# Optimization experiments

Hardware: AMD Instinct MI355X
Metric: run time of the kernel (lower is better)

The kernel has to match this reference:

```python
import jax, jax.numpy as jnp
import numpy as np

SCALE = 64 ** 0.5  # module hard-codes sqrt(64), independent of output_dim


def setup_inputs() -> dict:
    key = jax.random.key(0)
    kx, kw = jax.random.split(key)
    x = jax.random.normal(kx, (8, 2048, 768), dtype=jnp.float32)
    kernel = jax.random.normal(kw, (3, 768, 768), dtype=jnp.float32) * 0.02
    return {"x": x, "kernel": kernel}


def reference(x, kernel):
    # x: [b, s, d]; kernel: [3, d, o]
    q = jnp.einsum('bsd,do->bso', x, kernel[0])
    k = jnp.einsum('bsd,do->bso', x, kernel[1])
    v = jnp.einsum('bsd,do->bso', x, kernel[2])
    scores = jnp.einsum('bso,bto->bst', q, k) / SCALE  # [b, s, s]
    attn = jax.nn.softmax(scores, axis=-1)
    return jnp.einsum('bst,bto->bso', attn, v)
```

## Files before the change

### kernel.cpp

```cpp
#include <hip/hip_runtime.h>

typedef unsigned short u16;
typedef unsigned int   u32;
typedef __bf16  bf16x8 __attribute__((ext_vector_type(8)));
typedef float   f32x4  __attribute__((ext_vector_type(4)));

__device__ __forceinline__ u16 f2bf(float f) {
  u32 u = __builtin_bit_cast(u32, f);
  u += 0x7FFFu + ((u >> 16) & 1u);
  return (u16)(u >> 16);
}
__device__ __forceinline__ u16 to_bits(float f) { return f2bf(f); }
__device__ __forceinline__ u16 to_bits(u16 u)   { return u; }
__device__ __forceinline__ u32 pack2(float lo, float hi) {
  return (u32)f2bf(lo) | ((u32)f2bf(hi) << 16);
}

__device__ __forceinline__ void gload_lds16(const u16* g, u16* l) {
  __builtin_amdgcn_global_load_lds((const __attribute__((address_space(1))) void*)g,
                                   (__attribute__((address_space(3))) void*)l,
                                   16, 0, 0);
}

__global__ __launch_bounds__(256) void cvt_bf16(const float* __restrict__ in,
                                                u16* __restrict__ out) {
  size_t i = (size_t)blockIdx.x * 256 + threadIdx.x;
  const float4* in4 = (const float4*)in;
  float4 a = in4[2 * i], b = in4[2 * i + 1];
  uint4 o;
  o.x = pack2(a.x, a.y); o.y = pack2(a.z, a.w);
  o.z = pack2(b.x, b.y); o.w = pack2(b.z, b.w);
  ((uint4*)out)[i] = o;
}

template <typename InT>
__global__ __launch_bounds__(256) void transpose_bf16(const InT* __restrict__ in,
                                                      u16* __restrict__ out,
                                                      int R, int C, int in_ld,
                                                      size_t zin, size_t zout) {
  __shared__ u16 t[64][65];
  const InT* iz = in + (size_t)blockIdx.z * zin;
  u16* oz = out + (size_t)blockIdx.z * zout;
  const int tx = threadIdx.x & 63, ty = threadIdx.x >> 6;
  const int r0 = blockIdx.y * 64, c0 = blockIdx.x * 64;
#pragma unroll
  for (int rr = ty; rr < 64; rr += 4)
    t[rr][tx] = to_bits(iz[(size_t)(r0 + rr) * in_ld + c0 + tx]);
  __syncthreads();
#pragma unroll
  for (int rr = ty; rr < 64; rr += 4)
    oz[(size_t)(c0 + rr) * R + r0 + tx] = t[tx][rr];
}

template <int MODE, typename CT>
__global__ __launch_bounds__(256, 2)
void gemm_bt(const u16* __restrict__ A, const u16* __restrict__ B,
             CT* __restrict__ C, int Kd, int lda, int ldb, int ldc,
             size_t strideA, size_t strideB, size_t strideC,
             float* __restrict__ lsum) {
  __shared__ __align__(16) u16 sA[128 * 64];
  __shared__ __align__(16) u16 sB[128 * 64];

  const u32 gx = gridDim.x, gy = gridDim.y;
  const u32 lin = blockIdx.x + gx * (blockIdx.y + gy * blockIdx.z);
  const u32 nblk = gx * gy * gridDim.z;
  const u32 newlin = (lin & 7u) * (nblk >> 3) + (lin >> 3);
  const u32 bx = newlin % gx;
  const u32 tmp = newlin / gx;
  const u32 by = tmp % gy;
  const u32 bz = tmp / gy;

  const u16* Az = A + (size_t)bz * strideA;
  const u16* Bz = B + (size_t)bz * strideB;
  const int m0 = by * 128;
  int n0 = bx * 128;
  CT* Cz;
  if (MODE == 3) {
    Cz = C + (size_t)(n0 / 768) * strideC;
    n0 = n0 % 768;
  } else {
    Cz = C + (size_t)bz * strideC;
  }

  const int tid = threadIdx.x;
  const int lane = tid & 63, wave = tid >> 6;
  const int wm = (wave >> 1) * 64, wn = (wave & 1) * 64;
  const int lr = lane & 15, quad = lane >> 4;

  const u16* gA = Az + (size_t)(by * 128) * lda;
  const u16* gB = Bz + (size_t)(bx * 128) * ldb;
  const int stRow = wave * 8 + (lane >> 3);
  const int stCol = ((lane & 7) ^ (lane >> 3)) << 3;

  f32x4 acc[4][4] = {};

  for (int k0 = 0; k0 < Kd; k0 += 64) {
#pragma unroll
    for (int r = 0; r < 4; ++r) {
      gload_lds16(gA + (size_t)(stRow + r * 32) * lda + (k0 + stCol),
                  (u16*)((char*)sA + r * 4096 + wave * 1024));
      gload_lds16(gB + (size_t)(stRow + r * 32) * ldb + (k0 + stCol),
                  (u16*)((char*)sB + r * 4096 + wave * 1024));
    }
    __syncthreads();
#pragma unroll
    for (int kc = 0; kc < 2; ++kc) {
      bf16x8 af[4], bfv[4];
      const int coff = (((kc << 2) + quad) ^ (lr & 7)) << 4;
#pragma unroll
      for (int t = 0; t < 4; ++t) {
        af[t]  = *(const bf16x8*)((const char*)sA + (wm + t * 16 + lr) * 128 + coff);
        bfv[t] = *(const bf16x8*)((const char*)sB + (wn + t * 16 + lr) * 128 + coff);
      }
#pragma unroll
      for (int mt = 0; mt < 4; ++mt)
#pragma unroll
        for (int nt = 0; nt < 4; ++nt)
          acc[mt][nt] = __builtin_amdgcn_mfma_f32_16x16x32_bf16(
              af[mt], bfv[nt], acc[mt][nt], 0, 0, 0);
    }
    __syncthreads();
  }

  if (MODE == 1) {
    float* rowsum = (float*)sA;
    if (tid < 128) rowsum[tid] = 0.f;
    __syncthreads();
#pragma unroll
    for (int mt = 0; mt < 4; ++mt) {
#pragma unroll
      for (int i = 0; i < 4; ++i) {
        const int row_l = wm + mt * 16 + quad * 4 + i;
        CT* cp = Cz + (size_t)(m0 + row_l) * ldc + (n0 + wn + lr);
        float e[4], s = 0.f;
#pragma unroll
        for (int nt = 0; nt < 4; ++nt) {
          e[nt] = __expf(acc[mt][nt][i] * 0.125f);
          s += e[nt];
          cp[nt * 16] = f2bf(e[nt]);
        }
        s += __shfl_xor(s, 1);  s += __shfl_xor(s, 2);
        s += __shfl_xor(s, 4);  s += __shfl_xor(s, 8);
        if (lr == 0) atomicAdd(&rowsum[row_l], s);
      }
    }
    __syncthreads();
    if (tid < 128)
      lsum[(size_t)bx * 16384 + (size_t)bz * 2048 + m0 + tid] = rowsum[tid];
  } else if (MODE == 2) {
    float* rinv = (float*)sA;
    if (tid < 128) {
      float s = 0.f;
      const size_t base = (size_t)bz * 2048 + m0 + tid;
#pragma unroll
      for (int xt = 0; xt < 16; ++xt) s += lsum[(size_t)xt * 16384 + base];
      rinv[tid] = 1.0f / s;
    }
    __syncthreads();
#pragma unroll
    for (int mt = 0; mt < 4; ++mt) {
#pragma unroll
      for (int i = 0; i < 4; ++i) {
        const int row_l = wm + mt * 16 + quad * 4 + i;
        const float iv = rinv[row_l];
        CT* cp = Cz + (size_t)(m0 + row_l) * ldc + (n0 + wn + lr);
#pragma unroll
        for (int nt = 0; nt < 4; ++nt) cp[nt * 16] = acc[mt][nt][i] * iv;
      }
    }
  } else {
#pragma unroll
    for (int mt = 0; mt < 4; ++mt) {
#pragma unroll
      for (int i = 0; i < 4; ++i) {
        const int row_l = wm + mt * 16 + quad * 4 + i;
        CT* cp = Cz + (size_t)(m0 + row_l) * ldc + (n0 + wn + lr);
#pragma unroll
        for (int nt = 0; nt < 4; ++nt) {
          const float v = acc[mt][nt][i];
          if constexpr (sizeof(CT) == 2) cp[nt * 16] = f2bf(v);
          else                           cp[nt * 16] = v;
        }
      }
    }
  }
}

extern "C" void kernel_launch(void* const* d_in, const int* in_sizes, int n_in,
                              void* d_out, int out_size, void* d_ws, size_t ws_size,
                              hipStream_t stream) {
  const float* x = (const float*)d_in[0];
  const float* w = (const float*)d_in[1];
  float* out = (float*)d_out;
  char* ws = (char*)d_ws;

  const size_t NS = (size_t)16384 * 768;
  u16* Sc = (u16*)ws;
  u16* Xb = (u16*)ws;
  u16* Wt = (u16*)(ws + NS * 2);
  u16* Qm = (u16*)(ws + 67108864);
  u16* Km = Qm + NS;
  u16* Vm = Km + NS;
  float* Lpart = (float*)(ws + 117440512);
  u16* Vt = (u16*)(ws + 142606336);

  cvt_bf16<<<6144, 256, 0, stream>>>(x, Xb);
  transpose_bf16<float><<<dim3(12, 12, 3), 256, 0, stream>>>(
      w, Wt, 768, 768, 768, (size_t)768 * 768, (size_t)768 * 768);
  gemm_bt<3, u16><<<dim3(18, 128, 1), 256, 0, stream>>>(
      Xb, Wt, Qm, 768, 768, 768, 768, (size_t)0, (size_t)0, NS, nullptr);
  transpose_bf16<u16><<<dim3(12, 32, 8), 256, 0, stream>>>(
      Vm, Vt, 2048, 768, 768, (size_t)2048 * 768, (size_t)768 * 2048);
  gemm_bt<1, u16><<<dim3(16, 16, 8), 256, 0, stream>>>(
      Qm, Km, Sc, 768, 768, 768, 2048, (size_t)2048 * 768, (size_t)2048 * 768,
      (size_t)2048 * 2048, Lpart);
  gemm_bt<2, float><<<dim3(6, 16, 8), 256, 0, stream>>>(
      Sc, Vt, out, 2048, 2048, 2048, 768, (size_t)2048 * 2048,
      (size_t)768 * 2048, (size_t)2048 * 768, Lpart);
}
```

Baseline: 294.2 us.

## Fuse V transpose into QKV GEMM epilogue and merge prep kernels

The V projection tiles are now transposed through shared memory in the QKV GEMM epilogue and written directly to the transposed V buffer. This drops the separate transpose kernel and the intermediate V round trip through memory. The input conversion and weight transpose are combined into a single launch to cut launch overhead. The cost is a more complex epilogue with an extra barrier for the V-producing blocks, and branch divergence by block in the prep kernel.

Result: faster. 283.8 us (-3.5%).

```diff
diff --git a/kernel.cpp b/kernel.cpp
--- a/kernel.cpp
+++ b/kernel.cpp
@@ -2,6 +2,7 @@
 
 typedef unsigned short u16;
 typedef unsigned int   u32;
+typedef unsigned long long u64;
 typedef __bf16  bf16x8 __attribute__((ext_vector_type(8)));
 typedef float   f32x4  __attribute__((ext_vector_type(4)));
 
@@ -10,8 +11,6 @@
   u += 0x7FFFu + ((u >> 16) & 1u);
   return (u16)(u >> 16);
 }
-__device__ __forceinline__ u16 to_bits(float f) { return f2bf(f); }
-__device__ __forceinline__ u16 to_bits(u16 u)   { return u; }
 __device__ __forceinline__ u32 pack2(float lo, float hi) {
   return (u32)f2bf(lo) | ((u32)f2bf(hi) << 16);
 }
@@ -22,34 +21,34 @@
                                    16, 0, 0);
 }
 
-__global__ __launch_bounds__(256) void cvt_bf16(const float* __restrict__ in,
-                                                u16* __restrict__ out) {
-  size_t i = (size_t)blockIdx.x * 256 + threadIdx.x;
-  const float4* in4 = (const float4*)in;
-  float4 a = in4[2 * i], b = in4[2 * i + 1];
-  uint4 o;
-  o.x = pack2(a.x, a.y); o.y = pack2(a.z, a.w);
-  o.z = pack2(b.x, b.y); o.w = pack2(b.z, b.w);
-  ((uint4*)out)[i] = o;
-}
-
-template <typename InT>
-__global__ __launch_bounds__(256) void transpose_bf16(const InT* __restrict__ in,
-                                                      u16* __restrict__ out,
-                                                      int R, int C, int in_ld,
-                                                      size_t zin, size_t zout) {
-  __shared__ u16 t[64][65];
-  const InT* iz = in + (size_t)blockIdx.z * zin;
-  u16* oz = out + (size_t)blockIdx.z * zout;
-  const int tx = threadIdx.x & 63, ty = threadIdx.x >> 6;
-  const int r0 = blockIdx.y * 64, c0 = blockIdx.x * 64;
-#pragma unroll
-  for (int rr = ty; rr < 64; rr += 4)
-    t[rr][tx] = to_bits(iz[(size_t)(r0 + rr) * in_ld + c0 + tx]);
-  __syncthreads();
-#pragma unroll
-  for (int rr = ty; rr < 64; rr += 4)
-    oz[(size_t)(c0 + rr) * R + r0 + tx] = t[tx][rr];
+__global__ __launch_bounds__(256) void prep(const float* __restrict__ x,
+                                            const float* __restrict__ w,
+                                            u16* __restrict__ Xb,
+                                            u16* __restrict__ Wt) {
+  if (blockIdx.z < 3) {
+    if (blockIdx.x >= 12 || blockIdx.y >= 12) return;
+    __shared__ u16 t[64][65];
+    const float* iz = w + (size_t)blockIdx.z * 768 * 768;
+    u16* oz = Wt + (size_t)blockIdx.z * 768 * 768;
+    const int tx = threadIdx.x & 63, ty = threadIdx.x >> 6;
+    const int r0 = blockIdx.y * 64, c0 = blockIdx.x * 64;
+#pragma unroll
+    for (int rr = ty; rr < 64; rr += 4)
+      t[rr][tx] = f2bf(iz[(size_t)(r0 + rr) * 768 + c0 + tx]);
+    __syncthreads();
+#pragma unroll
+    for (int rr = ty; rr < 64; rr += 4)
+      oz[(size_t)(c0 + rr) * 768 + r0 + tx] = t[tx][rr];
+  } else {
+    const size_t lin = (size_t)(blockIdx.z - 3) * 256 + blockIdx.y * 16 + blockIdx.x;
+    const size_t i = lin * 256 + threadIdx.x;
+    const float4* in4 = (const float4*)x;
+    float4 a = in4[2 * i], b = in4[2 * i + 1];
+    uint4 o;
+    o.x = pack2(a.x, a.y); o.y = pack2(a.z, a.w);
+    o.z = pack2(b.x, b.y); o.w = pack2(b.z, b.w);
+    ((uint4*)Xb)[i] = o;
+  }
 }
 
 template <int MODE, typename CT>
@@ -57,9 +56,10 @@
 void gemm_bt(const u16* __restrict__ A, const u16* __restrict__ B,
              CT* __restrict__ C, int Kd, int lda, int ldb, int ldc,
              size_t strideA, size_t strideB, size_t strideC,
-             float* __restrict__ lsum) {
-  __shared__ __align__(16) u16 sA[128 * 64];
-  __shared__ __align__(16) u16 sB[128 * 64];
+             float* __restrict__ lsum, u16* __restrict__ vtp) {
+  __shared__ __align__(16) u16 sh[2][128 * 64];
+  u16* sA = sh[0];
+  u16* sB = sh[1];
 
   const u32 gx = gridDim.x, gy = gridDim.y;
   const u32 lin = blockIdx.x + gx * (blockIdx.y + gy * blockIdx.z);
@@ -74,9 +74,11 @@
   const u16* Bz = B + (size_t)bz * strideB;
   const int m0 = by * 128;
   int n0 = bx * 128;
+  int matrix = 0;
   CT* Cz;
   if (MODE == 3) {
-    Cz = C + (size_t)(n0 / 768) * strideC;
+    matrix = n0 / 768;
+    Cz = C + (size_t)matrix * strideC;
     n0 = n0 % 768;
   } else {
     Cz = C + (size_t)bz * strideC;
@@ -168,6 +170,33 @@
         for (int nt = 0; nt < 4; ++nt) cp[nt * 16] = acc[mt][nt][i] * iv;
       }
     }
+  } else if (MODE == 3 && matrix == 2) {
+    u16* T = sh[0];
+#pragma unroll
+    for (int mt = 0; mt < 4; ++mt) {
+      const int rg = (wave >> 1) * 16 + mt * 4 + quad;
+#pragma unroll
+      for (int nt = 0; nt < 4; ++nt) {
+        const int col = wn + nt * 16 + lr;
+        u64 v = (u64)f2bf(acc[mt][nt][0])
+              | ((u64)f2bf(acc[mt][nt][1]) << 16)
+              | ((u64)f2bf(acc[mt][nt][2]) << 32)
+              | ((u64)f2bf(acc[mt][nt][3]) << 48);
+        *(u64*)((char*)T + col * 256 + ((rg ^ (col & 31)) << 3)) = v;
+      }
+    }
+    __syncthreads();
+    const int b = m0 >> 11;
+    const int t0 = (m0 & 2047) + (lane << 1);
+    const int n0v = n0;
+#pragma unroll
+    for (int it = 0; it < 32; ++it) {
+      const int col = it * 4 + wave;
+      const u32 val = *(const u32*)((char*)T + col * 256 +
+                                    (((lane >> 1) ^ (col & 31)) << 3) +
+                                    ((lane & 1) << 2));
+      *(u32*)(vtp + ((size_t)b * 768 + n0v + col) * 2048 + t0) = val;
+    }
   } else {
 #pragma unroll
     for (int mt = 0; mt < 4; ++mt) {
@@ -176,11 +205,7 @@
         const int row_l = wm + mt * 16 + quad * 4 + i;
         CT* cp = Cz + (size_t)(m0 + row_l) * ldc + (n0 + wn + lr);
 #pragma unroll
-        for (int nt = 0; nt < 4; ++nt) {
-          const float v = acc[mt][nt][i];
-          if constexpr (sizeof(CT) == 2) cp[nt * 16] = f2bf(v);
-          else                           cp[nt * 16] = v;
-        }
+        for (int nt = 0; nt < 4; ++nt) cp[nt * 16] = f2bf(acc[mt][nt][i]);
       }
     }
   }
@@ -200,21 +225,16 @@
   u16* Wt = (u16*)(ws + NS * 2);
   u16* Qm = (u16*)(ws + 67108864);
   u16* Km = Qm + NS;
-  u16* Vm = Km + NS;
   float* Lpart = (float*)(ws + 117440512);
   u16* Vt = (u16*)(ws + 142606336);
 
-  cvt_bf16<<<6144, 256, 0, stream>>>(x, Xb);
-  transpose_bf16<float><<<dim3(12, 12, 3), 256, 0, stream>>>(
-      w, Wt, 768, 768, 768, (size_t)768 * 768, (size_t)768 * 768);
+  prep<<<dim3(16, 16, 27), 256, 0, stream>>>(x, w, Xb, Wt);
   gemm_bt<3, u16><<<dim3(18, 128, 1), 256, 0, stream>>>(
-      Xb, Wt, Qm, 768, 768, 768, 768, (size_t)0, (size_t)0, NS, nullptr);
-  transpose_bf16<u16><<<dim3(12, 32, 8), 256, 0, stream>>>(
-      Vm, Vt, 2048, 768, 768, (size_t)2048 * 768, (size_t)768 * 2048);
+      Xb, Wt, Qm, 768, 768, 768, 768, (size_t)0, (size_t)0, NS, nullptr, Vt);
   gemm_bt<1, u16><<<dim3(16, 16, 8), 256, 0, stream>>>(
       Qm, Km, Sc, 768, 768, 768, 2048, (size_t)2048 * 768, (size_t)2048 * 768,
-      (size_t)2048 * 2048, Lpart);
+      (size_t)2048 * 2048, Lpart, nullptr);
   gemm_bt<2, float><<<dim3(6, 16, 8), 256, 0, stream>>>(
       Sc, Vt, out, 2048, 2048, 2048, 768, (size_t)2048 * 2048,
-      (size_t)768 * 2048, (size_t)2048 * 768, Lpart);
-}
+      (size_t)768 * 2048, (size_t)2048 * 768, Lpart, nullptr);
+}
```
